# Kernel optimization log

Hardware: AMD Instinct MI355X
Metric: run time of the kernel (lower is better)

## Reference

```python
import jax, jax.numpy as jnp
import numpy as np

B = 131072
H = 128
GF = 10  # global feature size
SENDERS = jnp.array([0, 1])    # directed path graph on 2 nodes
RECEIVERS = jnp.array([1, 0])


def setup_inputs() -> dict:
    key = jax.random.key(0)
    ks = jax.random.split(key, 10)
    s = lambda fan_in: 1.0 / np.sqrt(fan_in)
    return {
        "x": jax.random.normal(ks[0], (B, 4), jnp.float32),
        "u": jax.random.normal(ks[1], (B, 1), jnp.float32),
        "node_mean": jax.random.normal(ks[2], (2,), jnp.float32) * 0.1,
        "node_std": jnp.ones((2,), jnp.float32),
        "edge_mean": jax.random.normal(ks[3], (3,), jnp.float32) * 0.1,
        "edge_std": jnp.ones((3,), jnp.float32),
        "We1": jax.random.normal(ks[4], (17, H), jnp.float32) * s(17),
        "be1": jnp.zeros((H,), jnp.float32),
        "We2": jax.random.normal(ks[5], (H, H), jnp.float32) * s(H),
        "be2": jnp.zeros((H,), jnp.float32),
        "Wn1": jax.random.normal(ks[6], (GF + 2 + H, H), jnp.float32) * s(GF + 2 + H),
        "bn1": jnp.zeros((H,), jnp.float32),
        "Wn2": jax.random.normal(ks[7], (H, 2), jnp.float32) * s(H),
        "bn2": jnp.zeros((2,), jnp.float32),
    }


def _gn_step(x, u, node_mean, node_std, edge_mean, edge_std,
             We1, be1, We2, be2, Wn1, bn1, Wn2, bn2):
    b = x.shape[0]
    # load_graph_features: node k = [theta_k, v_k]; edge feat = [action, 0, 0]
    nodes = jnp.stack([x[:, [0, 2]], x[:, [1, 3]]], axis=1)          # [B,2,2]
    edges = jnp.concatenate(
        [jnp.broadcast_to(u[:, None, :], (b, 2, 1)),
         jnp.zeros((b, 2, 2), x.dtype)], axis=-1)                    # [B,2,3]
    glob = jnp.zeros((b, 2, GF), x.dtype)                            # zeros globals
    # in_normalizer
    nodes = (nodes - node_mean) / node_std
    edges = (edges - edge_mean) / edge_std
    # edge model: [global, sender, receiver, edge] -> H
    e_in = jnp.concatenate(
        [glob, nodes[:, SENDERS], nodes[:, RECEIVERS], edges], axis=-1)  # [B,2,17]
    e = jax.nn.relu(jnp.einsum('bef,fh->beh', e_in, We1) + be1)
    e = jax.nn.relu(jnp.einsum('beh,hk->bek', e, We2) + be2)         # [B,2,H]
    # aggregate incoming edge effects per node (sum over receivers)
    agg = jnp.zeros((b, 2, H), x.dtype).at[:, RECEIVERS].add(e)      # [B,2,H]
    # node model: [global, node, agg] -> 2
    n_in = jnp.concatenate([glob, nodes, agg], axis=-1)              # [B,2,140]
    hdd = jax.nn.relu(jnp.einsum('bnf,fh->bnh', n_in, Wn1) + bn1)
    delta = jnp.einsum('bnh,hk->bnk', hdd, Wn2) + bn2                # [B,2,2]
    # scatter: state idx k <- delta[:,k,0], idx k+2 <- delta[:,k,1]
    delta_state = jnp.concatenate([delta[:, :, 0], delta[:, :, 1]], axis=-1)  # [B,4]
    return x + delta_state


def reference(x, u, node_mean, node_std, edge_mean, edge_std,
              We1, be1, We2, be2, Wn1, bn1, Wn2, bn2):
    return _gn_step(x, u, node_mean, node_std, edge_mean, edge_std,
                    We1, be1, We2, be2, Wn1, bn1, Wn2, bn2)
```

## Files before the change

### kernel.cpp

```cpp
#include <hip/hip_runtime.h>


typedef __attribute__((ext_vector_type(8))) short bf16x8;
typedef __attribute__((ext_vector_type(4))) float f32x4;

union U4B { uint4 u; bf16x8 b; };

__device__ __forceinline__ unsigned short f2bf(float f) {
  union { float f; unsigned u; } v; v.f = f;
  return (unsigned short)((v.u + 0x7FFFu + ((v.u >> 16) & 1u)) >> 16);
}

__device__ __forceinline__ unsigned cvtpk(float lo, float hi) {
  unsigned r;
  asm("v_cvt_pk_bf16_f32 %0, %1, %2" : "=v"(r) : "v"(lo), "v"(hi));
  return r;
}

__host__ __device__ __forceinline__ int kperm(int k) {
  int kk = k >> 5, gg = (k >> 3) & 3, i = k & 7;
  return kk * 32 + (i >> 2) * 16 + gg * 4 + (i & 3);
}

__global__ void gn_prep(const float* __restrict__ We1, const float* __restrict__ be1,
                        const float* __restrict__ We2, const float* __restrict__ Wn1,
                        const float* __restrict__ bn1, const float* __restrict__ Wn2,
                        const float* __restrict__ be2,
                        unsigned short* __restrict__ wsA) {
  int t = blockIdx.x * 256 + threadIdx.x;
  if (t < 1024) {
    int j = t >> 3, k = t & 7;
    wsA[t] = f2bf((k < 7) ? We1[(10 + k) * 128 + j] : be1[j]);
  } else if (t < 2048) {
    int t2 = t - 1024; int j = t2 >> 3, c = t2 & 7;
    float v = (c == 0) ? Wn1[10 * 128 + j] : (c == 1) ? Wn1[11 * 128 + j]
            : (c == 2) ? bn1[j] : 0.0f;
    wsA[t] = f2bf(v);
  } else if (t < 4096) {
    int i = t - 2048; int jp = i >> 7, k = i & 127;
    wsA[t] = f2bf((jp < 2) ? Wn2[kperm(k) * 2 + jp] : 0.0f);
  } else if (t < 20480) {
    int t2 = t - 4096; int j = t2 >> 7, k = t2 & 127;
    wsA[t] = f2bf(We2[kperm(k) * 128 + j]);
  } else if (t < 36864) {
    int t2 = t - 20480; int j = t2 >> 7, k = t2 & 127;
    wsA[t] = f2bf(Wn1[(12 + kperm(k)) * 128 + j]);
  } else if (t < 36992) {
    ((float*)(wsA + 36864))[t - 36864] = be2[t - 36864];
  }
}

#define WTILES 8192
#define NWAVES 2048

__global__ __launch_bounds__(256) __attribute__((amdgpu_waves_per_eu(2, 2)))
void gn_main(
    const float* __restrict__ x, const float* __restrict__ u,
    const float* __restrict__ nmean, const float* __restrict__ nstd,
    const float* __restrict__ emean, const float* __restrict__ estd,
    const float* __restrict__ bn2,
    const unsigned short* __restrict__ wsA,
    float* __restrict__ out)
{
  __shared__ __align__(16) unsigned short a2T[128 * 128];
  __shared__ __align__(16) unsigned short a3T[128 * 128];
  __shared__ __align__(16) unsigned short aLDS[2048];

  const int tid  = threadIdx.x;
  const int lane = tid & 63;
  const int wid  = tid >> 6;
  const int c15  = lane & 15;
  const int g    = lane >> 4;
  const int sw15 = (c15 & 7) << 4;

  for (int t = tid; t < 2048; t += 256) {
    int j = t >> 4, c = t & 15;
    uint4 v2 = *(const uint4*)(wsA + 4096 + j * 128 + c * 8);
    *(uint4*)((char*)a2T + j * 256 + ((c * 16) ^ ((j & 7) << 4))) = v2;
    uint4 v3 = *(const uint4*)(wsA + 20480 + j * 128 + c * 8);
    *(uint4*)((char*)a3T + j * 256 + ((c * 16) ^ ((j & 7) << 4))) = v3;
  }
  for (int t = tid; t < 1024; t += 256)
    ((unsigned*)aLDS)[t] = ((const unsigned*)wsA)[t];

  bf16x8 A4f[4];
  #pragma unroll
  for (int kk = 0; kk < 4; ++kk)
    A4f[kk] = *(const bf16x8*)(wsA + 2048 + c15 * 128 + kk * 32 + g * 8);
  f32x4 be2f[8];
  {
    const float* be2p = (const float*)(wsA + 36864);
    #pragma unroll
    for (int m = 0; m < 8; ++m)
      be2f[m] = *(const f32x4*)(be2p + m * 16 + g * 4);
  }

  const float nm0 = nmean[0], nm1 = nmean[1];
  const float is0 = 1.0f / nstd[0], is1 = 1.0f / nstd[1];
  const float em0 = emean[0], ie0 = 1.0f / estd[0];
  const float cea1 = (0.0f - emean[1]) / estd[1];
  const float cea2 = (0.0f - emean[2]) / estd[2];
  const float bn20 = bn2[0], bn21 = bn2[1];
  const unsigned cpkw = cvtpk(cea2, 1.0f);

  auto buildB = [&](int wt_, int n_, unsigned& pks_, bf16x8& Bv_,
                    float& xs0_, float& xs1_) {
    float4 xv_ = (float4){0.f, 0.f, 0.f, 0.f};
    float  uv_ = 0.f;
    if (g == 0) {
      int b = wt_ * 16 + n_ * 8 + (c15 >> 1);
      xv_ = *(const float4*)(x + b * 4);
      uv_ = u[b];
    }
    xs0_ = (c15 & 1) ? xv_.y : xv_.x;
    xs1_ = (c15 & 1) ? xv_.w : xv_.z;
    uint4 bu = (uint4){0u, 0u, 0u, 0u};
    if (g == 0) {
      float a0 = (xv_.x - nm0) * is0, a1 = (xv_.z - nm1) * is1;
      float b0 = (xv_.y - nm0) * is0, b1 = (xv_.w - nm1) * is1;
      bool  e  = (c15 & 1);
      float s0 = e ? b0 : a0, s1 = e ? b1 : a1;
      float r0 = e ? a0 : b0, r1 = e ? a1 : b1;
      float ea0 = (uv_ - em0) * ie0;
      bu.x = cvtpk(s0, s1); bu.y = cvtpk(r0, r1);
      bu.z = cvtpk(ea0, cea1); bu.w = cpkw;
    }
    pks_ = bu.x;
    U4B t; t.u = bu; Bv_ = t.b;
  };

  auto packE = [&](const f32x4 (&a)[8], bf16x8 (&E)[4]) {
    #pragma unroll
    for (int kk = 0; kk < 4; ++kk) {
      f32x4 a0 = a[2 * kk], a1 = a[2 * kk + 1];
      uint4 e;
      e.x = cvtpk(fmaxf(a0[0], 0.f), fmaxf(a0[1], 0.f));
      e.y = cvtpk(fmaxf(a0[2], 0.f), fmaxf(a0[3], 0.f));
      e.z = cvtpk(fmaxf(a1[0], 0.f), fmaxf(a1[1], 0.f));
      e.w = cvtpk(fmaxf(a1[2], 0.f), fmaxf(a1[3], 0.f));
      U4B t; t.u = e; E[kk] = t.b;
    }
  };
  auto packEswap = [&](const f32x4 (&a)[8], bf16x8 (&E)[4]) {
    #pragma unroll
    for (int kk = 0; kk < 4; ++kk) {
      f32x4 a0 = a[2 * kk], a1 = a[2 * kk + 1];
      uint4 e;
      e.x = __shfl_xor(cvtpk(fmaxf(a0[0], 0.f), fmaxf(a0[1], 0.f)), 1, 64);
      e.y = __shfl_xor(cvtpk(fmaxf(a0[2], 0.f), fmaxf(a0[3], 0.f)), 1, 64);
      e.z = __shfl_xor(cvtpk(fmaxf(a1[0], 0.f), fmaxf(a1[1], 0.f)), 1, 64);
      e.w = __shfl_xor(cvtpk(fmaxf(a1[2], 0.f), fmaxf(a1[3], 0.f)), 1, 64);
      U4B t; t.u = e; E[kk] = t.b;
    }
  };

  __syncthreads();

  for (int wt = blockIdx.x * 4 + wid; wt < WTILES; wt += NWAVES) {
    const int rowbase = wt * 32;

    unsigned aoff = 0;
    asm volatile("" : "+v"(aoff));
    const char* aB  = (const char*)aLDS + aoff;
    const char* a2B = (const char*)a2T + aoff;
    const char* a3B = (const char*)a3T + aoff;

    unsigned pks[2]; bf16x8 Bv[2];
    float xs0[2], xs1[2];
    #pragma unroll
    for (int n = 0; n < 2; ++n)
      buildB(wt, n, pks[n], Bv[n], xs0[n], xs1[n]);

    f32x4 acc[2][8];

    #pragma unroll
    for (int m = 0; m < 8; ++m) {
      U4B ta; ta.u = *(const uint4*)(aB + (m * 16 + c15) * 16);
      #pragma unroll
      for (int n = 0; n < 2; ++n) {
        f32x4 z = (f32x4){0.f, 0.f, 0.f, 0.f};
        acc[n][m] = __builtin_amdgcn_mfma_f32_16x16x32_bf16(ta.b, Bv[n], z, 0, 0, 0);
      }
    }
    bf16x8 E1[2][4];
    #pragma unroll
    for (int n = 0; n < 2; ++n) packE(acc[n], E1[n]);

    #pragma unroll
    for (int m = 0; m < 8; ++m) {
      #pragma unroll
      for (int n = 0; n < 2; ++n) acc[n][m] = be2f[m];
    }
    #pragma unroll
    for (int kk = 0; kk < 4; ++kk)
      #pragma unroll
      for (int m = 0; m < 8; ++m) {
        U4B tf; tf.u = *(const uint4*)(a2B + (m * 16 + c15) * 256 + ((kk * 64 + g * 16) ^ sw15));
        #pragma unroll
        for (int n = 0; n < 2; ++n)
          acc[n][m] = __builtin_amdgcn_mfma_f32_16x16x32_bf16(tf.b, E1[n][kk], acc[n][m], 0, 0, 0);
      }
    bf16x8 E2[2][4];
    #pragma unroll
    for (int n = 0; n < 2; ++n) packEswap(acc[n], E2[n]);

    #pragma unroll
    for (int m = 0; m < 8; ++m)
      #pragma unroll
      for (int n = 0; n < 2; ++n)
        acc[n][m] = (f32x4){0.f, 0.f, 0.f, 0.f};
    #pragma unroll
    for (int kk = 0; kk < 4; ++kk)
      #pragma unroll
      for (int m = 0; m < 8; ++m) {
        U4B tf; tf.u = *(const uint4*)(a3B + (m * 16 + c15) * 256 + ((kk * 64 + g * 16) ^ sw15));
        #pragma unroll
        for (int n = 0; n < 2; ++n)
          acc[n][m] = __builtin_amdgcn_mfma_f32_16x16x32_bf16(tf.b, E2[n][kk], acc[n][m], 0, 0, 0);
      }
    {
      U4B t4[2];
      #pragma unroll
      for (int n = 0; n < 2; ++n) {
        uint4 b4 = (uint4){0u, 0u, 0u, 0u};
        if (g == 0) { b4.x = pks[n]; b4.y = 0x00003F80u; }
        t4[n].u = b4;
      }
      #pragma unroll
      for (int m = 0; m < 8; ++m) {
        U4B te; te.u = *(const uint4*)(aB + 2048 + (m * 16 + c15) * 16);
        #pragma unroll
        for (int n = 0; n < 2; ++n)
          acc[n][m] = __builtin_amdgcn_mfma_f32_16x16x32_bf16(te.b, t4[n].b, acc[n][m], 0, 0, 0);
      }
    }

    {
      #pragma unroll
      for (int n = 0; n < 2; ++n) {
        bf16x8 HD[4];
        packE(acc[n], HD);
        f32x4 a4 = (f32x4){0.f, 0.f, 0.f, 0.f};
        #pragma unroll
        for (int kk = 0; kk < 4; ++kk)
          a4 = __builtin_amdgcn_mfma_f32_16x16x32_bf16(A4f[kk], HD[kk], a4, 0, 0, 0);
        if (g == 0) {
          int gr = rowbase + n * 16 + c15;
          int bidx = gr >> 1, k = gr & 1;
          out[bidx * 4 + k]     = xs0[n] + a4[0] + bn20;
          out[bidx * 4 + k + 2] = xs1[n] + a4[1] + bn21;
        }
      }
    }
  }
}

extern "C" void kernel_launch(void* const* d_in, const int* in_sizes, int n_in,
                              void* d_out, int out_size, void* d_ws, size_t ws_size,
                              hipStream_t stream) {
  const float* x   = (const float*)d_in[0];
  const float* u   = (const float*)d_in[1];
  const float* nm  = (const float*)d_in[2];
  const float* ns  = (const float*)d_in[3];
  const float* em  = (const float*)d_in[4];
  const float* es  = (const float*)d_in[5];
  const float* We1 = (const float*)d_in[6];
  const float* be1 = (const float*)d_in[7];
  const float* We2 = (const float*)d_in[8];
  const float* be2 = (const float*)d_in[9];
  const float* Wn1 = (const float*)d_in[10];
  const float* bn1 = (const float*)d_in[11];
  const float* Wn2 = (const float*)d_in[12];
  const float* bn2 = (const float*)d_in[13];
  unsigned short* wsA = (unsigned short*)d_ws;
  float* out = (float*)d_out;

  gn_prep<<<145, 256, 0, stream>>>(We1, be1, We2, Wn1, bn1, Wn2, be2, wsA);
  gn_main<<<512, 256, 0, stream>>>(x, u, nm, ns, em, es, bn2, wsA, out);
}
```

Measured before the change: 32.84 us.

## Move loop-invariant weights to LDS and software-pipeline LDS fragment loads

```diff
diff --git a/kernel.cpp b/kernel.cpp
--- a/kernel.cpp
+++ b/kernel.cpp
@@ -64,7 +64,7 @@
 {
   __shared__ __align__(16) unsigned short a2T[128 * 128];
   __shared__ __align__(16) unsigned short a3T[128 * 128];
-  __shared__ __align__(16) unsigned short aLDS[2048];
+  __shared__ __align__(16) unsigned short aLDS[4352];
 
   const int tid  = threadIdx.x;
   const int lane = tid & 63;
@@ -80,20 +80,10 @@
     uint4 v3 = *(const uint4*)(wsA + 20480 + j * 128 + c * 8);
     *(uint4*)((char*)a3T + j * 256 + ((c * 16) ^ ((j & 7) << 4))) = v3;
   }
-  for (int t = tid; t < 1024; t += 256)
+  for (int t = tid; t < 2048; t += 256)
     ((unsigned*)aLDS)[t] = ((const unsigned*)wsA)[t];
-
-  bf16x8 A4f[4];
-  #pragma unroll
-  for (int kk = 0; kk < 4; ++kk)
-    A4f[kk] = *(const bf16x8*)(wsA + 2048 + c15 * 128 + kk * 32 + g * 8);
-  f32x4 be2f[8];
-  {
-    const float* be2p = (const float*)(wsA + 36864);
-    #pragma unroll
-    for (int m = 0; m < 8; ++m)
-      be2f[m] = *(const f32x4*)(be2p + m * 16 + g * 4);
-  }
+  for (int t = tid; t < 128; t += 256)
+    ((unsigned*)aLDS)[2048 + t] = ((const unsigned*)(wsA + 36864))[t];
 
   const float nm0 = nmean[0], nm1 = nmean[1];
   const float is0 = 1.0f / nstd[0], is1 = 1.0f / nstd[1];
@@ -129,29 +119,69 @@
     U4B t; t.u = bu; Bv_ = t.b;
   };
 
-  auto packE = [&](const f32x4 (&a)[8], bf16x8 (&E)[4]) {
-    #pragma unroll
-    for (int kk = 0; kk < 4; ++kk) {
-      f32x4 a0 = a[2 * kk], a1 = a[2 * kk + 1];
-      uint4 e;
-      e.x = cvtpk(fmaxf(a0[0], 0.f), fmaxf(a0[1], 0.f));
-      e.y = cvtpk(fmaxf(a0[2], 0.f), fmaxf(a0[3], 0.f));
-      e.z = cvtpk(fmaxf(a1[0], 0.f), fmaxf(a1[1], 0.f));
-      e.w = cvtpk(fmaxf(a1[2], 0.f), fmaxf(a1[3], 0.f));
-      U4B t; t.u = e; E[kk] = t.b;
-    }
+  auto packE = [&](const f32x4 (&a)[2][8], bf16x8 (&E)[2][4]) {
+    #pragma unroll
+    for (int n = 0; n < 2; ++n)
+      #pragma unroll
+      for (int kk = 0; kk < 4; ++kk) {
+        f32x4 a0 = a[n][2 * kk], a1 = a[n][2 * kk + 1];
+        uint4 e;
+        e.x = cvtpk(fmaxf(a0[0], 0.f), fmaxf(a0[1], 0.f));
+        e.y = cvtpk(fmaxf(a0[2], 0.f), fmaxf(a0[3], 0.f));
+        e.z = cvtpk(fmaxf(a1[0], 0.f), fmaxf(a1[1], 0.f));
+        e.w = cvtpk(fmaxf(a1[2], 0.f), fmaxf(a1[3], 0.f));
+        U4B t; t.u = e; E[n][kk] = t.b;
+      }
   };
-  auto packEswap = [&](const f32x4 (&a)[8], bf16x8 (&E)[4]) {
-    #pragma unroll
-    for (int kk = 0; kk < 4; ++kk) {
-      f32x4 a0 = a[2 * kk], a1 = a[2 * kk + 1];
-      uint4 e;
-      e.x = __shfl_xor(cvtpk(fmaxf(a0[0], 0.f), fmaxf(a0[1], 0.f)), 1, 64);
-      e.y = __shfl_xor(cvtpk(fmaxf(a0[2], 0.f), fmaxf(a0[3], 0.f)), 1, 64);
-      e.z = __shfl_xor(cvtpk(fmaxf(a1[0], 0.f), fmaxf(a1[1], 0.f)), 1, 64);
-      e.w = __shfl_xor(cvtpk(fmaxf(a1[2], 0.f), fmaxf(a1[3], 0.f)), 1, 64);
-      U4B t; t.u = e; E[kk] = t.b;
-    }
+  auto packEswap = [&](const f32x4 (&a)[2][8], bf16x8 (&E)[2][4]) {
+    #pragma unroll
+    for (int n = 0; n < 2; ++n)
+      #pragma unroll
+      for (int kk = 0; kk < 4; ++kk) {
+        f32x4 a0 = a[n][2 * kk], a1 = a[n][2 * kk + 1];
+        uint4 e;
+        e.x = __shfl_xor(cvtpk(fmaxf(a0[0], 0.f), fmaxf(a0[1], 0.f)), 1, 64);
+        e.y = __shfl_xor(cvtpk(fmaxf(a0[2], 0.f), fmaxf(a0[3], 0.f)), 1, 64);
+        e.z = __shfl_xor(cvtpk(fmaxf(a1[0], 0.f), fmaxf(a1[1], 0.f)), 1, 64);
+        e.w = __shfl_xor(cvtpk(fmaxf(a1[2], 0.f), fmaxf(a1[3], 0.f)), 1, 64);
+        U4B t; t.u = e; E[n][kk] = t.b;
+      }
+  };
+
+  auto runLayer = [&](const char* base, const bf16x8 (&E)[2][4], f32x4 (&acc)[2][8]) {
+    U4B fA[8], fB[8];
+    #pragma unroll
+    for (int m = 0; m < 8; ++m)
+      fA[m].u = *(const uint4*)(base + (m * 16 + c15) * 256 + ((g * 16) ^ sw15));
+    #pragma unroll
+    for (int m = 0; m < 8; ++m)
+      fB[m].u = *(const uint4*)(base + (m * 16 + c15) * 256 + ((64 + g * 16) ^ sw15));
+    #pragma unroll
+    for (int m = 0; m < 8; ++m)
+      #pragma unroll
+      for (int n = 0; n < 2; ++n)
+        acc[n][m] = __builtin_amdgcn_mfma_f32_16x16x32_bf16(fA[m].b, E[n][0], acc[n][m], 0, 0, 0);
+    #pragma unroll
+    for (int m = 0; m < 8; ++m)
+      fA[m].u = *(const uint4*)(base + (m * 16 + c15) * 256 + ((128 + g * 16) ^ sw15));
+    #pragma unroll
+    for (int m = 0; m < 8; ++m)
+      #pragma unroll
+      for (int n = 0; n < 2; ++n)
+        acc[n][m] = __builtin_amdgcn_mfma_f32_16x16x32_bf16(fB[m].b, E[n][1], acc[n][m], 0, 0, 0);
+    #pragma unroll
+    for (int m = 0; m < 8; ++m)
+      fB[m].u = *(const uint4*)(base + (m * 16 + c15) * 256 + ((192 + g * 16) ^ sw15));
+    #pragma unroll
+    for (int m = 0; m < 8; ++m)
+      #pragma unroll
+      for (int n = 0; n < 2; ++n)
+        acc[n][m] = __builtin_amdgcn_mfma_f32_16x16x32_bf16(fA[m].b, E[n][2], acc[n][m], 0, 0, 0);
+    #pragma unroll
+    for (int m = 0; m < 8; ++m)
+      #pragma unroll
+      for (int n = 0; n < 2; ++n)
+        acc[n][m] = __builtin_amdgcn_mfma_f32_16x16x32_bf16(fB[m].b, E[n][3], acc[n][m], 0, 0, 0);
   };
 
   __syncthreads();
@@ -165,6 +195,11 @@
     const char* a2B = (const char*)a2T + aoff;
     const char* a3B = (const char*)a3T + aoff;
 
+    U4B A1t[8];
+    #pragma unroll
+    for (int m = 0; m < 8; ++m)
+      A1t[m].u = *(const uint4*)(aB + (m * 16 + c15) * 16);
+
     unsigned pks[2]; bf16x8 Bv[2];
     float xs0[2], xs1[2];
     #pragma unroll
@@ -174,50 +209,30 @@
     f32x4 acc[2][8];
 
     #pragma unroll
-    for (int m = 0; m < 8; ++m) {
-      U4B ta; ta.u = *(const uint4*)(aB + (m * 16 + c15) * 16);
+    for (int m = 0; m < 8; ++m)
       #pragma unroll
       for (int n = 0; n < 2; ++n) {
         f32x4 z = (f32x4){0.f, 0.f, 0.f, 0.f};
-        acc[n][m] = __builtin_amdgcn_mfma_f32_16x16x32_bf16(ta.b, Bv[n], z, 0, 0, 0);
-      }
-    }
+        acc[n][m] = __builtin_amdgcn_mfma_f32_16x16x32_bf16(A1t[m].b, Bv[n], z, 0, 0, 0);
+      }
     bf16x8 E1[2][4];
-    #pragma unroll
-    for (int n = 0; n < 2; ++n) packE(acc[n], E1[n]);
+    packE(acc, E1);
 
     #pragma unroll
     for (int m = 0; m < 8; ++m) {
-      #pragma unroll
-      for (int n = 0; n < 2; ++n) acc[n][m] = be2f[m];
-    }
-    #pragma unroll
-    for (int kk = 0; kk < 4; ++kk)
-      #pragma unroll
-      for (int m = 0; m < 8; ++m) {
-        U4B tf; tf.u = *(const uint4*)(a2B + (m * 16 + c15) * 256 + ((kk * 64 + g * 16) ^ sw15));
-        #pragma unroll
-        for (int n = 0; n < 2; ++n)
-          acc[n][m] = __builtin_amdgcn_mfma_f32_16x16x32_bf16(tf.b, E1[n][kk], acc[n][m], 0, 0, 0);
-      }
+      f32x4 bz = *(const f32x4*)(aB + 8192 + (m * 16 + g * 4) * 4);
+      acc[0][m] = bz; acc[1][m] = bz;
+    }
+    runLayer(a2B, E1, acc);
     bf16x8 E2[2][4];
-    #pragma unroll
-    for (int n = 0; n < 2; ++n) packEswap(acc[n], E2[n]);
-
-    #pragma unroll
-    for (int m = 0; m < 8; ++m)
-      #pragma unroll
-      for (int n = 0; n < 2; ++n)
-        acc[n][m] = (f32x4){0.f, 0.f, 0.f, 0.f};
-    #pragma unroll
-    for (int kk = 0; kk < 4; ++kk)
-      #pragma unroll
-      for (int m = 0; m < 8; ++m) {
-        U4B tf; tf.u = *(const uint4*)(a3B + (m * 16 + c15) * 256 + ((kk * 64 + g * 16) ^ sw15));
-        #pragma unroll
-        for (int n = 0; n < 2; ++n)
-          acc[n][m] = __builtin_amdgcn_mfma_f32_16x16x32_bf16(tf.b, E2[n][kk], acc[n][m], 0, 0, 0);
-      }
+    packEswap(acc, E2);
+
+    #pragma unroll
+    for (int m = 0; m < 8; ++m) {
+      acc[0][m] = (f32x4){0.f, 0.f, 0.f, 0.f};
+      acc[1][m] = (f32x4){0.f, 0.f, 0.f, 0.f};
+    }
+    runLayer(a3B, E2, acc);
     {
       U4B t4[2];
       #pragma unroll
@@ -236,14 +251,27 @@
     }
 
     {
+      U4B A4f[4];
+      #pragma unroll
+      for (int kk = 0; kk < 4; ++kk)
+        A4f[kk].u = *(const uint4*)(aB + 4096 + c15 * 256 + kk * 64 + g * 16);
       #pragma unroll
       for (int n = 0; n < 2; ++n) {
         bf16x8 HD[4];
-        packE(acc[n], HD);
+        #pragma unroll
+        for (int kk = 0; kk < 4; ++kk) {
+          f32x4 a0 = acc[n][2 * kk], a1 = acc[n][2 * kk + 1];
+          uint4 e;
+          e.x = cvtpk(fmaxf(a0[0], 0.f), fmaxf(a0[1], 0.f));
+          e.y = cvtpk(fmaxf(a0[2], 0.f), fmaxf(a0[3], 0.f));
+          e.z = cvtpk(fmaxf(a1[0], 0.f), fmaxf(a1[1], 0.f));
+          e.w = cvtpk(fmaxf(a1[2], 0.f), fmaxf(a1[3], 0.f));
+          U4B t; t.u = e; HD[kk] = t.b;
+        }
         f32x4 a4 = (f32x4){0.f, 0.f, 0.f, 0.f};
         #pragma unroll
         for (int kk = 0; kk < 4; ++kk)
-          a4 = __builtin_amdgcn_mfma_f32_16x16x32_bf16(A4f[kk], HD[kk], a4, 0, 0, 0);
+          a4 = __builtin_amdgcn_mfma_f32_16x16x32_bf16(A4f[kk].b, HD[kk], a4, 0, 0, 0);
         if (g == 0) {
           int gr = rowbase + n * 16 + c15;
           int bidx = gr >> 1, k = gr & 1;
```

Result: faster. 32.09 us (-2.3%).
